# Optimization experiments

Measured on AMD Instinct MI355X. Metric: run time of the kernel, lower is better.

Reference implementation:

```python
import jax, jax.numpy as jnp
import numpy as np

A_NUM = 9
C_NUM = 20


def generate_anchor(anc, grid):
    # anc: (A,2) w,h ; grid: (B,H,W,2) centers -> anchors (B,A,H,W,4)
    centers = grid[:, None]                      # (B,1,H,W,2)
    half = anc.reshape(1, -1, 1, 1, 2) * 0.5     # (1,A,1,1,2)
    return jnp.concatenate([centers - half, centers + half], axis=-1)


def iou_matrix(proposals, bboxes):
    # proposals: (B,A,H,W,4) -> (B,K,4); bboxes: (B,N,5)
    B = proposals.shape[0]
    p = proposals.reshape(B, -1, 4)[:, :, None, :]   # (B,K,1,4)
    bb = bboxes[:, None, :, :]                       # (B,1,N,5)
    s_p = (p[..., 2] - p[..., 0]) * (p[..., 3] - p[..., 1])
    s_b = (bb[..., 2] - bb[..., 0]) * (bb[..., 3] - bb[..., 1])
    ix1 = jnp.maximum(p[..., 0], bb[..., 0])
    iy1 = jnp.maximum(p[..., 1], bb[..., 1])
    ix2 = jnp.minimum(p[..., 2], bb[..., 2])
    iy2 = jnp.minimum(p[..., 3], bb[..., 3])
    s_i = jnp.clip(ix2 - ix1, 0.0) * jnp.clip(iy2 - iy1, 0.0)
    s_u = s_p + s_b - s_i
    iou = jnp.clip(s_i / (s_u + 1e-8), 0.0)
    invalid = (s_u <= 0) | (s_p <= 0) | (s_b <= 0) | (bb[..., 0] < 0)
    return jnp.where(invalid, 0.0, iou)              # (B,K,N)


def extract_anchor_data(anchor_data, idx):
    # anchor_data: (B,A,D,H,W) -> flat (B*A*H*W, D) -> gather
    B, A, D, H, W = anchor_data.shape
    flat = jnp.transpose(anchor_data, (0, 1, 3, 4, 2)).reshape(-1, D)
    return flat[idx]


def extract_class_scores(all_scores, idx, num_anchors):
    # all_scores: (B,C,H,W) -> (B,A,H,W,C) flat -> gather
    B, C, H, W = all_scores.shape
    s = jnp.transpose(all_scores, (0, 2, 3, 1))[:, None]          # (B,1,H,W,C)
    s = jnp.broadcast_to(s, (B, num_anchors, H, W, C)).reshape(-1, C)
    return s[idx]


def setup_inputs() -> dict:
    key = jax.random.key(0)
    ks = jax.random.split(key, 8)
    B, Cin, H, W = 32, 1280, 28, 28
    N, M = 64, 4096
    hid, out_ch = 128, 5 * A_NUM + C_NUM
    features = jax.random.normal(ks[0], (B, Cin, H, W), dtype=jnp.float32)
    # grid of feature-cell centers (GenerateGrid-style)
    xs = jnp.arange(W, dtype=jnp.float32) + 0.5
    ys = jnp.arange(H, dtype=jnp.float32) + 0.5
    gx, gy = jnp.meshgrid(xs, ys, indexing='xy')
    grid = jnp.broadcast_to(jnp.stack([gx, gy], axis=-1), (B, H, W, 2))
    anc = jnp.array([[1.0, 1], [2, 2], [3, 3], [4, 4], [5, 5], [2, 3], [3, 2], [3, 5], [5, 3]], dtype=jnp.float32)
    tl = jax.random.uniform(ks[1], (B, N, 2), minval=0.0, maxval=20.0)
    wh = jax.random.uniform(ks[2], (B, N, 2), minval=1.0, maxval=8.0)
    cls = jax.random.randint(ks[3], (B, N, 1), 0, C_NUM).astype(jnp.float32)
    bb = jnp.concatenate([tl, tl + wh, cls], axis=-1)
    valid = jax.random.uniform(ks[4], (B, N, 1)) > 0.25
    bboxes = jnp.where(valid, bb, -1.0)
    K = B * A_NUM * H * W
    pos_anchor_idx = jax.random.randint(ks[5], (M,), 0, K, dtype=jnp.int64 if jax.config.jax_enable_x64 else jnp.int32)
    neg_anchor_idx = jax.random.randint(ks[6], (M,), 0, K, dtype=pos_anchor_idx.dtype)
    W1 = jax.random.normal(ks[7], (hid, Cin), dtype=jnp.float32) * 0.02
    b1 = jnp.zeros((hid,), dtype=jnp.float32)
    W2 = jax.random.normal(jax.random.fold_in(key, 99), (out_ch, hid), dtype=jnp.float32) * 0.02
    b2 = jnp.zeros((out_ch,), dtype=jnp.float32)
    return {"features": features, "grid": grid, "anc": anc, "bboxes": bboxes,
            "pos_anchor_idx": pos_anchor_idx, "neg_anchor_idx": neg_anchor_idx,
            "W1": W1, "b1": b1, "W2": W2, "b2": b2}


def reference(features, grid, anc, bboxes, pos_anchor_idx, neg_anchor_idx, W1, b1, W2, b2):
    B, Cin, H, W = features.shape
    A, C = A_NUM, C_NUM
    # anchors + broadcast IoU matrix
    anchors = generate_anchor(anc, grid)                 # (B,A,H,W,4)
    iou_mat = iou_matrix(anchors, bboxes)                # (B,A*H*W,N)
    # prediction head: 1x1 conv -> (dropout eval: identity) -> leaky_relu -> 1x1 conv
    h = jnp.einsum('bchw,oc->bohw', features, W1) + b1[None, :, None, None]
    h = jax.nn.leaky_relu(h, negative_slope=0.01)
    out = jnp.einsum('bchw,oc->bohw', h, W2) + b2[None, :, None, None]  # (B,5A+C,H,W)
    anchor_raw = out[:, :5 * A].reshape(B, A, 5, H, W)
    conf_sq = jax.nn.sigmoid(anchor_raw[:, :, 0:1])      # (B,A,1,H,W)
    off_raw = anchor_raw[:, :, 1:]                       # (B,A,4,H,W)
    off_sq = jnp.concatenate([jax.nn.sigmoid(off_raw[:, :, :2]) - 0.5, off_raw[:, :, 2:]], axis=2)
    class_raw = out[:, 5 * A:]                           # (B,C,H,W)
    # training path: irregular gathers
    class_scores = extract_class_scores(class_raw, pos_anchor_idx, A)   # (M,C)
    offsets = extract_anchor_data(off_sq, pos_anchor_idx)               # (M,4)
    conf_pos = extract_anchor_data(conf_sq, pos_anchor_idx)             # (M,1)
    conf_neg = extract_anchor_data(conf_sq, neg_anchor_idx)             # (M,1)
    conf_scores = jnp.concatenate([conf_pos, conf_neg], axis=0)         # (2M,1)
    return conf_scores, offsets, class_scores, iou_mat
```

## Files before the change

kernel.cpp:

```cpp
#include <hip/hip_runtime.h>
#include <cstdint>

#define A_NUM 9
#define C_NUM 20
#define B_SZ 32
#define HW 784
#define P_NUM (A_NUM*HW)
#define NBOX 64
#define CIN 1280
#define HID 128
#define M_IDX 4096
#define KS_ALL 40
#define ASTR 40
#define HSTR 136
#define OSTR 80
#define IOU_PB 64

#define CONF_OFF 0
#define OFFS_OFF (2*M_IDX)
#define CLS_OFF  (OFFS_OFF + 4*M_IDX)
#define IOU_OFF  (CLS_OFF + C_NUM*M_IDX)

#define GEMM_BLKS (13*B_SZ)
#define IOU_BX ((P_NUM + IOU_PB - 1)/IOU_PB)
#define IOU_BLKS (IOU_BX*B_SZ)

typedef short bf16x8 __attribute__((ext_vector_type(8)));
typedef float f32x4  __attribute__((ext_vector_type(4)));

__device__ __forceinline__ unsigned pack_bf16(float lo, float hi) {
  unsigned a = __builtin_bit_cast(unsigned, lo);
  unsigned b = __builtin_bit_cast(unsigned, hi);
  return ((a + 0x8000u) >> 16) | ((b + 0x8000u) & 0xffff0000u);
}

__global__ __launch_bounds__(256) void prep_w(const float* __restrict__ W1,
                                              const float* __restrict__ W2,
                                              uint4* __restrict__ W1f,
                                              uint4* __restrict__ W2f) {
  int id = blockIdx.x * 256 + threadIdx.x;
  if (id < 20480) {
    int lane = id & 63;
    int ntile = (id >> 6) & 7;
    int ks = id >> 9;
    int lo = lane & 15, quad = lane >> 4;
    int n = ntile * 16 + lo;
    int k0 = ks * 32 + quad * 8;
    const float* src = W1 + n * CIN + k0;
    float4 x = *(const float4*)src;
    float4 y = *(const float4*)(src + 4);
    uint4 p;
    p.x = pack_bf16(x.x, x.y);
    p.y = pack_bf16(x.z, x.w);
    p.z = pack_bf16(y.x, y.y);
    p.w = pack_bf16(y.z, y.w);
    W1f[id] = p;
  } else {
    int i2 = id - 20480;
    int lane = i2 & 63;
    int ntile = (i2 >> 6) % 5;
    int ks = i2 / 320;
    int lo = lane & 15, quad = lane >> 4;
    int n = ntile * 16 + lo;
    int k0 = ks * 32 + quad * 8;
    uint4 p = (uint4){0, 0, 0, 0};
    if (n < 5 * A_NUM + C_NUM) {
      const float* src = W2 + n * HID + k0;
      float4 x = *(const float4*)src;
      float4 y = *(const float4*)(src + 4);
      p.x = pack_bf16(x.x, x.y);
      p.y = pack_bf16(x.z, x.w);
      p.z = pack_bf16(y.x, y.y);
      p.w = pack_bf16(y.z, y.w);
    }
    W2f[i2] = p;
  }
}

union SharedU {
  struct { unsigned short Asm[2][64 * ASTR]; } g;
  struct { unsigned short hs[64 * HSTR]; } e;
  struct { float sb[NBOX * 5]; float4 sp4[IOU_PB]; } i;
};

__global__ __launch_bounds__(256) void fused_main(
    const float* __restrict__ F, const unsigned short* __restrict__ W1f,
    const unsigned short* __restrict__ W2f, const float* __restrict__ b1,
    const float* __restrict__ b2, float* __restrict__ Hd,
    const float* __restrict__ gridc, const float* __restrict__ anc,
    const float* __restrict__ bboxes, float* __restrict__ iou_out) {
  __shared__ SharedU sh;
  const int bid = blockIdx.x;
  const int t = threadIdx.x;

  if (bid >= GEMM_BLKS) {
    const int bid2 = bid - GEMM_BLKS;
    const int b = bid2 / IOU_BX;
    const int p0 = (bid2 - b * IOU_BX) * IOU_PB;
    float* sb = sh.i.sb;
    float4* sp4 = sh.i.sp4;
    for (int i = t; i < NBOX * 5; i += 256) sb[i] = bboxes[b * NBOX * 5 + i];
    if (t < IOU_PB) {
      int p = p0 + t;
      float x1 = 0.f, y1 = 0.f, x2 = 0.f, y2 = 0.f;
      if (p < P_NUM) {
        int a = p / HW, hw = p - a * HW;
        float2 c = ((const float2*)gridc)[b * HW + hw];
        float hx = anc[a * 2 + 0] * 0.5f, hy = anc[a * 2 + 1] * 0.5f;
        x1 = c.x - hx; y1 = c.y - hy; x2 = c.x + hx; y2 = c.y + hy;
      }
      sp4[t] = make_float4(x1, y1, x2, y2);
    }
    __syncthreads();
    const int nl = (t & 15) * 4;
    const int pi = t >> 4;
#pragma unroll
    for (int ip = 0; ip < 4; ip++) {
      const int pl = pi + 16 * ip;
      const int p = p0 + pl;
      const float4 pb = sp4[pl];
      const float spA = (pb.z - pb.x) * (pb.w - pb.y);
      float4 res;
#pragma unroll
      for (int jn = 0; jn < 4; jn++) {
        const int n = nl + jn;
        float bx1 = sb[n * 5 + 0], by1 = sb[n * 5 + 1];
        float bx2 = sb[n * 5 + 2], by2 = sb[n * 5 + 3];
        float s_b = (bx2 - bx1) * (by2 - by1);
        float ix1 = fmaxf(pb.x, bx1), iy1 = fmaxf(pb.y, by1);
        float ix2 = fminf(pb.z, bx2), iy2 = fminf(pb.w, by2);
        float si = fmaxf(ix2 - ix1, 0.f) * fmaxf(iy2 - iy1, 0.f);
        float su = spA + s_b - si;
        float iou = fmaxf(si / (su + 1e-8f), 0.f);
        bool invalid = (su <= 0.f) | (spA <= 0.f) | (s_b <= 0.f) | (bx1 < 0.f);
        float v = invalid ? 0.f : iou;
        if (jn == 0) res.x = v; else if (jn == 1) res.y = v;
        else if (jn == 2) res.z = v; else res.w = v;
      }
      if (p < P_NUM)
        *(float4*)&iou_out[((size_t)(b * P_NUM + p)) * 64 + nl] = res;
    }
    return;
  }

  const int b = bid / 13;
  const int m0 = (bid - b * 13) * 64;
  const int wave = t >> 6, lane = t & 63;
  const int quad = lane >> 4, lo = lane & 15;

  const int sm = t & 63;
  const int kh = t >> 6;
  const int gm = m0 + sm;
  const bool mval = gm < HW;
  const float* Fb = F + (size_t)b * CIN * HW + (mval ? gm : 0);

  f32x4 acc[4][2];
#pragma unroll
  for (int i = 0; i < 4; i++)
#pragma unroll
    for (int j = 0; j < 2; j++) acc[i][j] = (f32x4){0.f, 0.f, 0.f, 0.f};

  float va[8];
  uint4 vb[2][2];

  auto loadA = [&](int kk) {
    const int k0 = kk * 32 + kh * 8;
#pragma unroll
    for (int i = 0; i < 8; i++) va[i] = Fb[(size_t)(k0 + i) * HW];
  };
  auto loadB = [&](int kk, uint4* dst) {
    const unsigned short* g =
        W1f + (size_t)((kk * 8 + wave * 2) * 64 + lane) * 8;
    dst[0] = *(const uint4*)g;
    dst[1] = *(const uint4*)(g + 512);
  };
  auto stageA = [&](int buf) {
    uint4 p;
    if (mval) {
      p.x = pack_bf16(va[0], va[1]);
      p.y = pack_bf16(va[2], va[3]);
      p.z = pack_bf16(va[4], va[5]);
      p.w = pack_bf16(va[6], va[7]);
    } else {
      p = (uint4){0, 0, 0, 0};
    }
    *(uint4*)&sh.g.Asm[buf][sm * ASTR + kh * 8] = p;
  };
  auto compute = [&](int buf, uint4* bv) {
    const unsigned short* Ab = &sh.g.Asm[buf][lo * ASTR + quad * 8];
    bf16x8 af[4];
#pragma unroll
    for (int i = 0; i < 4; i++) af[i] = *(const bf16x8*)(Ab + i * 16 * ASTR);
    bf16x8 b0 = __builtin_bit_cast(bf16x8, bv[0]);
    bf16x8 b1v = __builtin_bit_cast(bf16x8, bv[1]);
#pragma unroll
    for (int i = 0; i < 4; i++) {
      acc[i][0] = __builtin_amdgcn_mfma_f32_16x16x32_bf16(af[i], b0, acc[i][0], 0, 0, 0);
      acc[i][1] = __builtin_amdgcn_mfma_f32_16x16x32_bf16(af[i], b1v, acc[i][1], 0, 0, 0);
    }
  };

  loadA(0);
  loadB(0, vb[0]);
  stageA(0);
  __syncthreads();
  for (int kk = 0; kk < KS_ALL; kk++) {
    const int cur = kk & 1;
    if (kk + 1 < KS_ALL) {
      loadA(kk + 1);
      loadB(kk + 1, vb[cur ^ 1]);
    }
    compute(cur, vb[cur]);
    if (kk + 1 < KS_ALL) stageA(cur ^ 1);
    __syncthreads();
  }

  {
    const float bias0 = b1[wave * 32 + lo];
    const float bias1 = b1[wave * 32 + 16 + lo];
    unsigned short* hs = sh.e.hs;
#pragma unroll
    for (int i = 0; i < 4; i++) {
#pragma unroll
      for (int j = 0; j < 2; j++) {
        const int n = wave * 32 + j * 16 + lo;
        const float bias = j ? bias1 : bias0;
#pragma unroll
        for (int r = 0; r < 4; r++) {
          float v = acc[i][j][r] + bias;
          v = v > 0.f ? v : 0.01f * v;
          const int m = i * 16 + quad * 4 + r;
          unsigned u = __builtin_bit_cast(unsigned, v);
          hs[m * HSTR + n] = (unsigned short)((u + 0x8000u) >> 16);
        }
      }
    }
  }
  __syncthreads();

  {
    f32x4 acc2[5];
#pragma unroll
    for (int nt = 0; nt < 5; nt++) acc2[nt] = (f32x4){0.f, 0.f, 0.f, 0.f};
    const unsigned short* hb = sh.e.hs + (wave * 16 + lo) * HSTR + quad * 8;
#pragma unroll
    for (int ks = 0; ks < 4; ks++) {
      bf16x8 af = *(const bf16x8*)(hb + ks * 32);
#pragma unroll
      for (int nt = 0; nt < 5; nt++) {
        bf16x8 bf = *(const bf16x8*)(W2f + (size_t)((ks * 5 + nt) * 64 + lane) * 8);
        acc2[nt] = __builtin_amdgcn_mfma_f32_16x16x32_bf16(af, bf, acc2[nt], 0, 0, 0);
      }
    }
    const int mrow = m0 + wave * 16 + quad * 4;
#pragma unroll
    for (int nt = 0; nt < 5; nt++) {
      const int o = nt * 16 + lo;
      if (o < 5 * A_NUM + C_NUM) {
        const float bz = b2[o];
        const int t5 = (o < 5 * A_NUM) ? (o % 5) : 5;
#pragma unroll
        for (int r = 0; r < 4; r++) {
          const int m = mrow + r;
          if (m < HW) {
            float v = acc2[nt][r] + bz;
            if (t5 == 0) v = 1.f / (1.f + expf(-v));
            else if (t5 == 1 || t5 == 2) v = 1.f / (1.f + expf(-v)) - 0.5f;
            Hd[((size_t)b * HW + m) * OSTR + o] = v;
          }
        }
      }
    }
  }
}

__global__ __launch_bounds__(256) void gather2(
    const int* __restrict__ pos_idx, const int* __restrict__ neg_idx,
    const float* __restrict__ Hd, float* __restrict__ out) {
  const int bid = blockIdx.x;
  if (bid < M_IDX / 8) {
    const int g = threadIdx.x >> 5;
    const int l = threadIdx.x & 31;
    const int slot = bid * 8 + g;
    const int idx = pos_idx[slot];
    const int b = idx / P_NUM, r = idx - b * P_NUM;
    const int a = r / HW, hw = r - a * HW;
    const float* row = Hd + ((size_t)b * HW + hw) * OSTR;
    if (l == 0)       out[CONF_OFF + slot] = row[a * 5];
    else if (l < 5)   out[OFFS_OFF + slot * 4 + (l - 1)] = row[a * 5 + l];
    else if (l < 25)  out[CLS_OFF + slot * C_NUM + (l - 5)] = row[5 * A_NUM + (l - 5)];
  } else {
    const int tt = (bid - M_IDX / 8) * 256 + threadIdx.x;
    if (tt < M_IDX) {
      const int idx = neg_idx[tt];
      const int b = idx / P_NUM, r = idx - b * P_NUM;
      const int a = r / HW, hw = r - a * HW;
      out[CONF_OFF + M_IDX + tt] = Hd[((size_t)b * HW + hw) * OSTR + a * 5];
    }
  }
}

extern "C" void kernel_launch(void* const* d_in, const int* in_sizes, int n_in,
                              void* d_out, int out_size, void* d_ws, size_t ws_size,
                              hipStream_t stream) {
  const float* features = (const float*)d_in[0];
  const float* gridc    = (const float*)d_in[1];
  const float* anc      = (const float*)d_in[2];
  const float* bboxes   = (const float*)d_in[3];
  const int*   pos_idx  = (const int*)d_in[4];
  const int*   neg_idx  = (const int*)d_in[5];
  const float* W1       = (const float*)d_in[6];
  const float* b1       = (const float*)d_in[7];
  const float* W2       = (const float*)d_in[8];
  const float* b2       = (const float*)d_in[9];
  float* out = (float*)d_out;

  uint4* W1f = (uint4*)d_ws;
  uint4* W2f = (uint4*)((char*)d_ws + 327680);
  float* Hd  = (float*)((char*)d_ws + 327680 + 20480);

  hipLaunchKernelGGL(prep_w, dim3(85), dim3(256), 0, stream, W1, W2, W1f, W2f);
  hipLaunchKernelGGL(fused_main, dim3(GEMM_BLKS + IOU_BLKS), dim3(256), 0, stream,
                     features, (const unsigned short*)W1f,
                     (const unsigned short*)W2f, b1, b2, Hd,
                     gridc, anc, bboxes, out + IOU_OFF);
  hipLaunchKernelGGL(gather2, dim3(M_IDX / 8 + 16), dim3(256), 0, stream,
                     pos_idx, neg_idx, Hd, out);
}
```

Measured before the change: 284.3 us.

## Give each wave its own 16-row GEMM tile with register operands, no LDS staging

The first GEMM is restructured so each wave owns a 16-row M fragment across all 128 hidden columns. A fragments are loaded straight from global memory into registers and packed to bf16 there, replacing the shared-memory double buffer and the per-step block barriers. B fragments for all 8 N tiles are double-buffered in registers. The hidden activations go through per-wave fp32 LDS and are repacked to bf16 for the second GEMM. W1 traffic rises because every wave reloads the full weight slice, register pressure grows, and the grid becomes 392 GEMM blocks, which divides evenly since 784 = 49*16.

```diff
diff --git a/kernel.cpp b/kernel.cpp
--- a/kernel.cpp
+++ b/kernel.cpp
@@ -11,8 +11,7 @@
 #define HID 128
 #define M_IDX 4096
 #define KS_ALL 40
-#define ASTR 40
-#define HSTR 136
+#define HSF 132
 #define OSTR 80
 #define IOU_PB 64
 
@@ -21,7 +20,7 @@
 #define CLS_OFF  (OFFS_OFF + 4*M_IDX)
 #define IOU_OFF  (CLS_OFF + C_NUM*M_IDX)
 
-#define GEMM_BLKS (13*B_SZ)
+#define GEMM_BLKS 392
 #define IOU_BX ((P_NUM + IOU_PB - 1)/IOU_PB)
 #define IOU_BLKS (IOU_BX*B_SZ)
 
@@ -78,14 +77,13 @@
 }
 
 union SharedU {
-  struct { unsigned short Asm[2][64 * ASTR]; } g;
-  struct { unsigned short hs[64 * HSTR]; } e;
+  float hs[4][16 * HSF];
   struct { float sb[NBOX * 5]; float4 sp4[IOU_PB]; } i;
 };
 
 __global__ __launch_bounds__(256) void fused_main(
-    const float* __restrict__ F, const unsigned short* __restrict__ W1f,
-    const unsigned short* __restrict__ W2f, const float* __restrict__ b1,
+    const float* __restrict__ F, const uint4* __restrict__ W1f,
+    const uint4* __restrict__ W2f, const float* __restrict__ b1,
     const float* __restrict__ b2, float* __restrict__ Hd,
     const float* __restrict__ gridc, const float* __restrict__ anc,
     const float* __restrict__ bboxes, float* __restrict__ iou_out) {
@@ -143,96 +141,65 @@
     return;
   }
 
-  const int b = bid / 13;
-  const int m0 = (bid - b * 13) * 64;
-  const int wave = t >> 6, lane = t & 63;
+  const int w = t >> 6, lane = t & 63;
   const int quad = lane >> 4, lo = lane & 15;
-
-  const int sm = t & 63;
-  const int kh = t >> 6;
-  const int gm = m0 + sm;
-  const bool mval = gm < HW;
-  const float* Fb = F + (size_t)b * CIN * HW + (mval ? gm : 0);
-
-  f32x4 acc[4][2];
-#pragma unroll
-  for (int i = 0; i < 4; i++)
-#pragma unroll
-    for (int j = 0; j < 2; j++) acc[i][j] = (f32x4){0.f, 0.f, 0.f, 0.f};
-
-  float va[8];
-  uint4 vb[2][2];
-
-  auto loadA = [&](int kk) {
-    const int k0 = kk * 32 + kh * 8;
-#pragma unroll
-    for (int i = 0; i < 8; i++) va[i] = Fb[(size_t)(k0 + i) * HW];
+  const int g = bid * 4 + w;
+  const int b = g / 49;
+  const int mf = g - b * 49;
+  const int m0 = mf * 16;
+
+  const float* Fq = F + (size_t)b * CIN * HW + (size_t)quad * 8 * HW + m0 + lo;
+
+  f32x4 acc[8];
+#pragma unroll
+  for (int i = 0; i < 8; i++) acc[i] = (f32x4){0.f, 0.f, 0.f, 0.f};
+
+  float va0[8], va1[8];
+  uint4 vb0[8], vb1[8];
+
+  auto loadA = [&](int kk, float* va) {
+    const float* p = Fq + (size_t)kk * 32 * HW;
+#pragma unroll
+    for (int j = 0; j < 8; j++) va[j] = p[(size_t)j * HW];
   };
-  auto loadB = [&](int kk, uint4* dst) {
-    const unsigned short* g =
-        W1f + (size_t)((kk * 8 + wave * 2) * 64 + lane) * 8;
-    dst[0] = *(const uint4*)g;
-    dst[1] = *(const uint4*)(g + 512);
+  auto loadB = [&](int kk, uint4* vb) {
+    const uint4* p = W1f + (size_t)kk * 512 + lane;
+#pragma unroll
+    for (int nf = 0; nf < 8; nf++) vb[nf] = p[nf * 64];
   };
-  auto stageA = [&](int buf) {
-    uint4 p;
-    if (mval) {
-      p.x = pack_bf16(va[0], va[1]);
-      p.y = pack_bf16(va[2], va[3]);
-      p.z = pack_bf16(va[4], va[5]);
-      p.w = pack_bf16(va[6], va[7]);
-    } else {
-      p = (uint4){0, 0, 0, 0};
-    }
-    *(uint4*)&sh.g.Asm[buf][sm * ASTR + kh * 8] = p;
+  auto step = [&](const float* va, const uint4* vb) {
+    uint4 ap;
+    ap.x = pack_bf16(va[0], va[1]);
+    ap.y = pack_bf16(va[2], va[3]);
+    ap.z = pack_bf16(va[4], va[5]);
+    ap.w = pack_bf16(va[6], va[7]);
+    bf16x8 af = __builtin_bit_cast(bf16x8, ap);
+#pragma unroll
+    for (int nf = 0; nf < 8; nf++)
+      acc[nf] = __builtin_amdgcn_mfma_f32_16x16x32_bf16(
+          af, __builtin_bit_cast(bf16x8, vb[nf]), acc[nf], 0, 0, 0);
   };
-  auto compute = [&](int buf, uint4* bv) {
-    const unsigned short* Ab = &sh.g.Asm[buf][lo * ASTR + quad * 8];
-    bf16x8 af[4];
-#pragma unroll
-    for (int i = 0; i < 4; i++) af[i] = *(const bf16x8*)(Ab + i * 16 * ASTR);
-    bf16x8 b0 = __builtin_bit_cast(bf16x8, bv[0]);
-    bf16x8 b1v = __builtin_bit_cast(bf16x8, bv[1]);
-#pragma unroll
-    for (int i = 0; i < 4; i++) {
-      acc[i][0] = __builtin_amdgcn_mfma_f32_16x16x32_bf16(af[i], b0, acc[i][0], 0, 0, 0);
-      acc[i][1] = __builtin_amdgcn_mfma_f32_16x16x32_bf16(af[i], b1v, acc[i][1], 0, 0, 0);
-    }
-  };
-
-  loadA(0);
-  loadB(0, vb[0]);
-  stageA(0);
-  __syncthreads();
-  for (int kk = 0; kk < KS_ALL; kk++) {
-    const int cur = kk & 1;
-    if (kk + 1 < KS_ALL) {
-      loadA(kk + 1);
-      loadB(kk + 1, vb[cur ^ 1]);
-    }
-    compute(cur, vb[cur]);
-    if (kk + 1 < KS_ALL) stageA(cur ^ 1);
-    __syncthreads();
+
+  loadA(0, va0); loadB(0, vb0);
+  loadA(1, va1); loadB(1, vb1);
+#pragma unroll 2
+  for (int kk = 0; kk < KS_ALL; kk += 2) {
+    step(va0, vb0);
+    if (kk + 2 < KS_ALL) { loadA(kk + 2, va0); loadB(kk + 2, vb0); }
+    step(va1, vb1);
+    if (kk + 3 < KS_ALL) { loadA(kk + 3, va1); loadB(kk + 3, vb1); }
   }
 
   {
-    const float bias0 = b1[wave * 32 + lo];
-    const float bias1 = b1[wave * 32 + 16 + lo];
-    unsigned short* hs = sh.e.hs;
-#pragma unroll
-    for (int i = 0; i < 4; i++) {
-#pragma unroll
-      for (int j = 0; j < 2; j++) {
-        const int n = wave * 32 + j * 16 + lo;
-        const float bias = j ? bias1 : bias0;
-#pragma unroll
-        for (int r = 0; r < 4; r++) {
-          float v = acc[i][j][r] + bias;
-          v = v > 0.f ? v : 0.01f * v;
-          const int m = i * 16 + quad * 4 + r;
-          unsigned u = __builtin_bit_cast(unsigned, v);
-          hs[m * HSTR + n] = (unsigned short)((u + 0x8000u) >> 16);
-        }
+    float* hsw = sh.hs[w];
+#pragma unroll
+    for (int nf = 0; nf < 8; nf++) {
+      const float bb = b1[nf * 16 + lo];
+#pragma unroll
+      for (int r = 0; r < 4; r++) {
+        float v = acc[nf][r] + bb;
+        v = v > 0.f ? v : 0.01f * v;
+        hsw[(quad * 4 + r) * HSF + nf * 16 + lo] = v;
       }
     }
   }
@@ -242,17 +209,27 @@
     f32x4 acc2[5];
 #pragma unroll
     for (int nt = 0; nt < 5; nt++) acc2[nt] = (f32x4){0.f, 0.f, 0.f, 0.f};
-    const unsigned short* hb = sh.e.hs + (wave * 16 + lo) * HSTR + quad * 8;
+    const float* hrow = sh.hs[w] + lo * HSF + quad * 8;
 #pragma unroll
     for (int ks = 0; ks < 4; ks++) {
-      bf16x8 af = *(const bf16x8*)(hb + ks * 32);
+      const float* hp = hrow + ks * 32;
+      float2 p0 = *(const float2*)(hp + 0);
+      float2 p1 = *(const float2*)(hp + 2);
+      float2 p2 = *(const float2*)(hp + 4);
+      float2 p3 = *(const float2*)(hp + 6);
+      uint4 ap;
+      ap.x = pack_bf16(p0.x, p0.y);
+      ap.y = pack_bf16(p1.x, p1.y);
+      ap.z = pack_bf16(p2.x, p2.y);
+      ap.w = pack_bf16(p3.x, p3.y);
+      bf16x8 af = __builtin_bit_cast(bf16x8, ap);
 #pragma unroll
       for (int nt = 0; nt < 5; nt++) {
-        bf16x8 bf = *(const bf16x8*)(W2f + (size_t)((ks * 5 + nt) * 64 + lane) * 8);
+        bf16x8 bf = __builtin_bit_cast(bf16x8, W2f[(ks * 5 + nt) * 64 + lane]);
         acc2[nt] = __builtin_amdgcn_mfma_f32_16x16x32_bf16(af, bf, acc2[nt], 0, 0, 0);
       }
     }
-    const int mrow = m0 + wave * 16 + quad * 4;
+    const int mrow = m0 + quad * 4;
 #pragma unroll
     for (int nt = 0; nt < 5; nt++) {
       const int o = nt * 16 + lo;
@@ -262,12 +239,10 @@
 #pragma unroll
         for (int r = 0; r < 4; r++) {
           const int m = mrow + r;
-          if (m < HW) {
-            float v = acc2[nt][r] + bz;
-            if (t5 == 0) v = 1.f / (1.f + expf(-v));
-            else if (t5 == 1 || t5 == 2) v = 1.f / (1.f + expf(-v)) - 0.5f;
-            Hd[((size_t)b * HW + m) * OSTR + o] = v;
-          }
+          float v = acc2[nt][r] + bz;
+          if (t5 == 0) v = 1.f / (1.f + expf(-v));
+          else if (t5 == 1 || t5 == 2) v = 1.f / (1.f + expf(-v)) - 0.5f;
+          Hd[((size_t)b * HW + m) * OSTR + o] = v;
         }
       }
     }
@@ -321,8 +296,7 @@
 
   hipLaunchKernelGGL(prep_w, dim3(85), dim3(256), 0, stream, W1, W2, W1f, W2f);
   hipLaunchKernelGGL(fused_main, dim3(GEMM_BLKS + IOU_BLKS), dim3(256), 0, stream,
-                     features, (const unsigned short*)W1f,
-                     (const unsigned short*)W2f, b1, b2, Hd,
+                     features, W1f, W2f, b1, b2, Hd,
                      gridc, anc, bboxes, out + IOU_OFF);
   hipLaunchKernelGGL(gather2, dim3(M_IDX / 8 + 16), dim3(256), 0, stream,
                      pos_idx, neg_idx, Hd, out);
```

Measured after the change: 261.4 us. 8.1% less time.
